# Performance work log

Hardware: AMD Instinct MI355X
Metric: run time of the kernel (lower is better)

Reference implementation:

```python
import jax, jax.numpy as jnp
import numpy as np


def _iir_forward(b_coeff, rho, psi, u_in, y_init, u_init):
    # Coefficient computation: stable 2nd-order resonator parameterization
    r = jax.nn.sigmoid(rho)
    theta = jnp.pi * jax.nn.sigmoid(psi)
    a1 = -2.0 * r * jnp.cos(theta)
    a2 = r * r

    B, T = u_in.shape
    nb = b_coeff.shape[0]  # number of FIR taps (n_b)

    # FIR (moving-average) part, fully vectorized over batch and time:
    # v[t] = sum_k b[k] * u[t-k]; past inputs come from u_init = [u[-1], u[-2], ...]
    u_ext = jnp.concatenate([u_init[:, ::-1], u_in], axis=1)  # [B, T + nb - 1], time-ordered
    v = jnp.zeros_like(u_in)
    for k in range(nb):  # small fixed loop over filter taps
        v = v + b_coeff[k] * jax.lax.dynamic_slice_in_dim(u_ext, nb - 1 - k, T, axis=1)

    # AR (recursive) part: y[t] = v[t] - a1*y[t-1] - a2*y[t-2]  (sequential scan over time)
    def step(carry, v_t):
        y1, y2 = carry  # y[t-1], y[t-2], each [B]
        y = v_t - a1 * y1 - a2 * y2
        return (y, y1), y

    init = (y_init[:, 0], y_init[:, 1])  # [y[-1], y[-2]] per lfiltic convention
    _, y = jax.lax.scan(step, init, v.T)  # y: [T, B]
    return y.T  # [B, T]


def setup_inputs() -> dict:
    key = jax.random.key(0)
    k1, k2, k3, k4 = jax.random.split(key, 4)
    B, T, NB = 1024, 16384, 3
    return {
        "b_coeff": 0.1 * jax.random.normal(k1, (NB,), dtype=jnp.float32),
        "rho": jnp.asarray(jax.random.normal(k2, (), dtype=jnp.float32) + 0.9),
        "psi": jnp.asarray(jax.random.normal(k3, (), dtype=jnp.float32) * 0.5),
        "u_in": jax.random.normal(k4, (B, T), dtype=jnp.float32),
        "y_init": jnp.zeros((B, 2), dtype=jnp.float32),
        "u_init": jnp.zeros((B, NB - 1), dtype=jnp.float32),
    }


def reference(b_coeff, rho, psi, u_in, y_init, u_init):
    return _iir_forward(b_coeff, rho, psi, u_in, y_init, u_init)
```

## Files before the change

kernel.cpp:

```cpp
#include <hip/hip_runtime.h>
#include <math.h>


#define TLEN  16384
#define HALF  8192
#define NT    256
#define CK    32
#define NCH   256
#define CARRY (2*NCH)

__device__ __forceinline__ void mat2_sq(float& m00, float& m01, float& m10, float& m11) {
    float t00 = m00*m00 + m01*m10;
    float t01 = m00*m01 + m01*m11;
    float t10 = m10*m00 + m11*m10;
    float t11 = m10*m01 + m11*m11;
    m00 = t00; m01 = t01; m10 = t10; m11 = t11;
}

__global__ __launch_bounds__(NT, 4)
void iir_kernel(const float* __restrict__ bc,
                const float* __restrict__ rho_p,
                const float* __restrict__ psi_p,
                const float* __restrict__ u_in,
                const float* __restrict__ y_init,
                const float* __restrict__ u_init,
                float* __restrict__ y_out)
{
    __shared__ float sc[2*NCH + 2];
    const int row = blockIdx.x;
    const int tid = threadIdx.x;

    const float rho = rho_p[0];
    const float psi = psi_p[0];
    const float r   = 1.0f / (1.0f + expf(-rho));
    const float th  = 3.14159265358979323846f / (1.0f + expf(-psi));
    const float a1  = -2.0f * r * cosf(th);
    const float a2  = r * r;
    const float b0  = bc[0], b1 = bc[1], b2 = bc[2];

    const float* urow = u_in  + (size_t)row * TLEN;
    float*       orow = y_out + (size_t)row * TLEN;

    for (int h = 0; h < 2; ++h) {
        const float* uc0 = urow + h * HALF + CK * tid;

        float um2, um1;
        if (tid == 0 && h == 0) {
            um2 = u_init[2*row + 1];
            um1 = u_init[2*row + 0];
        } else {
            float2 ub = *(const float2*)(uc0 - 2);
            um2 = ub.x; um1 = ub.y;
        }

        float uu[CK];
        #pragma unroll
        for (int k = 0; k < CK/4; ++k)
            *(float4*)&uu[4*k] = ((const float4*)uc0)[k];

        float v[CK];
        float y1 = 0.0f, y2 = 0.0f;
        #pragma unroll
        for (int j = 0; j < CK; ++j) {
            float uc = uu[j];
            float vv = fmaf(b2, um2, fmaf(b1, um1, b0 * uc));
            v[j] = vv;
            float y = fmaf(-a1, y1, fmaf(-a2, y2, vv));
            y2 = y1; y1 = y;
            um2 = um1; um1 = uc;
        }
        sc[2*tid]     = y1;
        sc[2*tid + 1] = y2;
        __syncthreads();

        if (tid < 64) {
            const int l = tid;
            float m00 = -a1, m01 = -a2, m10 = 1.0f, m11 = 0.0f;
            #pragma unroll
            for (int s = 0; s < 5; ++s) mat2_sq(m00, m01, m10, m11);

            float da[4], db[4];
            #pragma unroll
            for (int m = 0; m < 4; ++m) {
                da[m] = sc[8*l + 2*m];
                db[m] = sc[8*l + 2*m + 1];
            }

            float seed0 = 0.0f, seed1 = 0.0f;
            if (l == 0) {
                if (h == 0) { seed0 = y_init[2*row]; seed1 = y_init[2*row + 1]; }
                else        { seed0 = sc[CARRY]; seed1 = sc[CARRY + 1]; }
            }
            float s0 = seed0, s1 = seed1;
            #pragma unroll
            for (int m = 0; m < 4; ++m) {
                float n0 = fmaf(m00, s0, fmaf(m01, s1, da[m]));
                float n1 = fmaf(m10, s0, fmaf(m11, s1, db[m]));
                s0 = n0; s1 = n1;
            }
            float w00 = m00, w01 = m01, w10 = m10, w11 = m11;
            mat2_sq(w00, w01, w10, w11);
            mat2_sq(w00, w01, w10, w11);
            #pragma unroll
            for (int p = 0; p < 6; ++p) {
                float o0 = __shfl_up(s0, 1 << p);
                float o1 = __shfl_up(s1, 1 << p);
                if (l >= (1 << p)) {
                    s0 = fmaf(w00, o0, fmaf(w01, o1, s0));
                    s1 = fmaf(w10, o0, fmaf(w11, o1, s1));
                }
                if (p < 5) mat2_sq(w00, w01, w10, w11);
            }
            float p0 = __shfl_up(s0, 1);
            float p1 = __shfl_up(s1, 1);
            if (l == 0) { p0 = seed0; p1 = seed1; }
            float c0 = p0, c1 = p1;
            #pragma unroll
            for (int m = 0; m < 4; ++m) {
                sc[2*(4*l + m)]     = c0;
                sc[2*(4*l + m) + 1] = c1;
                float n0 = fmaf(m00, c0, fmaf(m01, c1, da[m]));
                float n1 = fmaf(m10, c0, fmaf(m11, c1, db[m]));
                c0 = n0; c1 = n1;
            }
        }
        __syncthreads();

        float y1f = sc[2*tid];
        float y2f = sc[2*tid + 1];
        float* oc0 = orow + h * HALF + CK * tid;
        float yy[CK];
        #pragma unroll
        for (int j = 0; j < CK; ++j) {
            float y = fmaf(-a1, y1f, fmaf(-a2, y2f, v[j]));
            yy[j] = y;
            y2f = y1f; y1f = y;
        }
        #pragma unroll
        for (int k = 0; k < CK/4; ++k)
            ((float4*)oc0)[k] = *(const float4*)&yy[4*k];

        if (tid == NT - 1) {
            sc[CARRY]     = y1f;
            sc[CARRY + 1] = y2f;
        }
    }
}

extern "C" void kernel_launch(void* const* d_in, const int* in_sizes, int n_in,
                              void* d_out, int out_size, void* d_ws, size_t ws_size,
                              hipStream_t stream) {
    const float* bc    = (const float*)d_in[0];
    const float* rho   = (const float*)d_in[1];
    const float* psi   = (const float*)d_in[2];
    const float* u_in  = (const float*)d_in[3];
    const float* y_in  = (const float*)d_in[4];
    const float* u_ini = (const float*)d_in[5];
    float* y = (float*)d_out;
    const int B = in_sizes[3] / TLEN;
    iir_kernel<<<B, NT, 0, stream>>>(bc, rho, psi, u_in, y_in, u_ini, y);
}
```

Before: 133.5 us.

## Stage loads through padded per-wave LDS, use wave-level scan, and prefetch second half

Each wave now owns a contiguous 2048-element segment and stages global loads and stores through a padded per-wave LDS region, so global accesses become coalesced float4 streams instead of per-thread 128-byte strided chunks. The single-wave scan over all 256 chunk states is replaced by a wave-local shuffle scan in every wave plus a short 4-step cross-wave combine, and the per-lane matrix prefix powers are precomputed once. The second half's input is prefetched into registers while the first half computes. The cost is more registers (staged float4 buffer, matrices), extra LDS traffic, and reliance on __threadfence_block rather than barriers for intra-wave LDS visibility.

After: 146.6 us. 9.8% more time.

```diff
diff --git a/kernel.cpp b/kernel.cpp
--- a/kernel.cpp
+++ b/kernel.cpp
@@ -5,16 +5,21 @@
 #define TLEN  16384
 #define HALF  8192
 #define NT    256
-#define CK    32
-#define NCH   256
-#define CARRY (2*NCH)
+#define NW    4
+#define SEG   2048
+#define WPAD  2304
+#define SUMS  (NW * WPAD)
+#define CARRY (SUMS + 16)
+#define LDSF  (CARRY + 2)
 
-__device__ __forceinline__ void mat2_sq(float& m00, float& m01, float& m10, float& m11) {
-    float t00 = m00*m00 + m01*m10;
-    float t01 = m00*m01 + m01*m11;
-    float t10 = m10*m00 + m11*m10;
-    float t11 = m10*m01 + m11*m11;
-    m00 = t00; m01 = t01; m10 = t10; m11 = t11;
+struct M2 { float a, b, c, d; };
+__device__ __forceinline__ M2 mmul(const M2& x, const M2& y) {
+    M2 r;
+    r.a = fmaf(x.a, y.a, x.b * y.c);
+    r.b = fmaf(x.a, y.b, x.b * y.d);
+    r.c = fmaf(x.c, y.a, x.d * y.c);
+    r.d = fmaf(x.c, y.b, x.d * y.d);
+    return r;
 }
 
 __global__ __launch_bounds__(NT, 4)
@@ -26,9 +31,12 @@
                 const float* __restrict__ u_init,
                 float* __restrict__ y_out)
 {
-    __shared__ float sc[2*NCH + 2];
+    __shared__ __align__(16) float lds[LDSF];
     const int row = blockIdx.x;
     const int tid = threadIdx.x;
+    const int w   = tid >> 6;
+    const int l   = tid & 63;
+    float* wreg = lds + w * WPAD;
 
     const float rho = rho_p[0];
     const float psi = psi_p[0];
@@ -38,30 +46,55 @@
     const float a2  = r * r;
     const float b0  = bc[0], b1 = bc[1], b2 = bc[2];
 
+    M2 M = { -a1, -a2, 1.0f, 0.0f };
+    #pragma unroll
+    for (int s = 0; s < 5; ++s) M = mmul(M, M);
+    M2 W = M, P = { 1.0f, 0.0f, 0.0f, 1.0f };
+    #pragma unroll
+    for (int p = 0; p < 6; ++p) {
+        if ((l >> p) & 1) P = mmul(W, P);
+        W = mmul(W, W);
+    }
+    const M2 Mseg = W;
+
     const float* urow = u_in  + (size_t)row * TLEN;
     float*       orow = y_out + (size_t)row * TLEN;
 
+    float4 st[8];
+    {
+        const float4* us = (const float4*)(urow + w * SEG);
+        #pragma unroll
+        for (int k = 0; k < 8; ++k) st[k] = us[l + 64 * k];
+    }
+
     for (int h = 0; h < 2; ++h) {
-        const float* uc0 = urow + h * HALF + CK * tid;
+        #pragma unroll
+        for (int k = 0; k < 8; ++k) {
+            int g = l + 64 * k;
+            *(float4*)&wreg[4 * (g + (g >> 3))] = st[k];
+        }
+        __threadfence_block();
+
+        float uu[32];
+        #pragma unroll
+        for (int j = 0; j < 8; ++j)
+            *(float4*)&uu[4 * j] = *(const float4*)&wreg[4 * (9 * l + j)];
 
         float um2, um1;
-        if (tid == 0 && h == 0) {
-            um2 = u_init[2*row + 1];
-            um1 = u_init[2*row + 0];
-        } else {
-            float2 ub = *(const float2*)(uc0 - 2);
-            um2 = ub.x; um1 = ub.y;
+        {
+            float pm2 = __shfl_up(uu[30], 1);
+            float pm1 = __shfl_up(uu[31], 1);
+            if (l == 0) {
+                int gstart = h * HALF + w * SEG;
+                if (gstart == 0) { um2 = u_init[2 * row + 1]; um1 = u_init[2 * row + 0]; }
+                else { float2 b = *(const float2*)(urow + gstart - 2); um2 = b.x; um1 = b.y; }
+            } else { um2 = pm2; um1 = pm1; }
         }
 
-        float uu[CK];
-        #pragma unroll
-        for (int k = 0; k < CK/4; ++k)
-            *(float4*)&uu[4*k] = ((const float4*)uc0)[k];
-
-        float v[CK];
+        float v[32];
         float y1 = 0.0f, y2 = 0.0f;
         #pragma unroll
-        for (int j = 0; j < CK; ++j) {
+        for (int j = 0; j < 32; ++j) {
             float uc = uu[j];
             float vv = fmaf(b2, um2, fmaf(b1, um1, b0 * uc));
             v[j] = vv;
@@ -69,80 +102,72 @@
             y2 = y1; y1 = y;
             um2 = um1; um1 = uc;
         }
-        sc[2*tid]     = y1;
-        sc[2*tid + 1] = y2;
-        __syncthreads();
 
-        if (tid < 64) {
-            const int l = tid;
-            float m00 = -a1, m01 = -a2, m10 = 1.0f, m11 = 0.0f;
+        if (h == 0) {
+            const float4* us = (const float4*)(urow + HALF + w * SEG);
             #pragma unroll
-            for (int s = 0; s < 5; ++s) mat2_sq(m00, m01, m10, m11);
+            for (int k = 0; k < 8; ++k) st[k] = us[l + 64 * k];
+        }
 
-            float da[4], db[4];
-            #pragma unroll
-            for (int m = 0; m < 4; ++m) {
-                da[m] = sc[8*l + 2*m];
-                db[m] = sc[8*l + 2*m + 1];
-            }
-
-            float seed0 = 0.0f, seed1 = 0.0f;
-            if (l == 0) {
-                if (h == 0) { seed0 = y_init[2*row]; seed1 = y_init[2*row + 1]; }
-                else        { seed0 = sc[CARRY]; seed1 = sc[CARRY + 1]; }
-            }
-            float s0 = seed0, s1 = seed1;
-            #pragma unroll
-            for (int m = 0; m < 4; ++m) {
-                float n0 = fmaf(m00, s0, fmaf(m01, s1, da[m]));
-                float n1 = fmaf(m10, s0, fmaf(m11, s1, db[m]));
+        float s0 = y1, s1 = y2;
+        M2 Wp = M;
+        #pragma unroll
+        for (int p = 0; p < 6; ++p) {
+            float o0 = __shfl_up(s0, 1 << p);
+            float o1 = __shfl_up(s1, 1 << p);
+            if (l >= (1 << p)) {
+                float n0 = fmaf(Wp.a, o0, fmaf(Wp.b, o1, s0));
+                float n1 = fmaf(Wp.c, o0, fmaf(Wp.d, o1, s1));
                 s0 = n0; s1 = n1;
             }
-            float w00 = m00, w01 = m01, w10 = m10, w11 = m11;
-            mat2_sq(w00, w01, w10, w11);
-            mat2_sq(w00, w01, w10, w11);
-            #pragma unroll
-            for (int p = 0; p < 6; ++p) {
-                float o0 = __shfl_up(s0, 1 << p);
-                float o1 = __shfl_up(s1, 1 << p);
-                if (l >= (1 << p)) {
-                    s0 = fmaf(w00, o0, fmaf(w01, o1, s0));
-                    s1 = fmaf(w10, o0, fmaf(w11, o1, s1));
-                }
-                if (p < 5) mat2_sq(w00, w01, w10, w11);
-            }
-            float p0 = __shfl_up(s0, 1);
-            float p1 = __shfl_up(s1, 1);
-            if (l == 0) { p0 = seed0; p1 = seed1; }
-            float c0 = p0, c1 = p1;
-            #pragma unroll
-            for (int m = 0; m < 4; ++m) {
-                sc[2*(4*l + m)]     = c0;
-                sc[2*(4*l + m) + 1] = c1;
-                float n0 = fmaf(m00, c0, fmaf(m01, c1, da[m]));
-                float n1 = fmaf(m10, c0, fmaf(m11, c1, db[m]));
-                c0 = n0; c1 = n1;
-            }
+            if (p < 5) Wp = mmul(Wp, Wp);
+        }
+        float e0 = __shfl_up(s0, 1);
+        float e1 = __shfl_up(s1, 1);
+        if (l == 0) { e0 = 0.0f; e1 = 0.0f; }
+
+        if (l == 63) {
+            lds[SUMS + 8 * h + 2 * w]     = s0;
+            lds[SUMS + 8 * h + 2 * w + 1] = s1;
         }
         __syncthreads();
 
-        float y1f = sc[2*tid];
-        float y2f = sc[2*tid + 1];
-        float* oc0 = orow + h * HALF + CK * tid;
-        float yy[CK];
+        float t0, t1;
+        if (h == 0) { t0 = y_init[2 * row]; t1 = y_init[2 * row + 1]; }
+        else        { t0 = lds[CARRY]; t1 = lds[CARRY + 1]; }
+        float c0 = t0, c1 = t1;
         #pragma unroll
-        for (int j = 0; j < CK; ++j) {
-            float y = fmaf(-a1, y1f, fmaf(-a2, y2f, v[j]));
-            yy[j] = y;
-            y2f = y1f; y1f = y;
+        for (int j = 0; j < NW; ++j) {
+            float q0 = lds[SUMS + 8 * h + 2 * j];
+            float q1 = lds[SUMS + 8 * h + 2 * j + 1];
+            float n0 = fmaf(Mseg.a, c0, fmaf(Mseg.b, c1, q0));
+            float n1 = fmaf(Mseg.c, c0, fmaf(Mseg.d, c1, q1));
+            c0 = n0; c1 = n1;
+            if (j == w - 1) { t0 = c0; t1 = c1; }
         }
+        if (h == 0 && tid == 0) { lds[CARRY] = c0; lds[CARRY + 1] = c1; }
+
+        float in0 = fmaf(P.a, t0, fmaf(P.b, t1, e0));
+        float in1 = fmaf(P.c, t0, fmaf(P.d, t1, e1));
+
+        float py1 = in0, py2 = in1;
         #pragma unroll
-        for (int k = 0; k < CK/4; ++k)
-            ((float4*)oc0)[k] = *(const float4*)&yy[4*k];
+        for (int j = 0; j < 8; ++j) {
+            float x0 = fmaf(-a1, py1, fmaf(-a2, py2, v[4 * j + 0]));
+            float x1 = fmaf(-a1, x0,  fmaf(-a2, py1, v[4 * j + 1]));
+            float x2 = fmaf(-a1, x1,  fmaf(-a2, x0,  v[4 * j + 2]));
+            float x3 = fmaf(-a1, x2,  fmaf(-a2, x1,  v[4 * j + 3]));
+            float4 q; q.x = x0; q.y = x1; q.z = x2; q.w = x3;
+            *(float4*)&wreg[4 * (9 * l + j)] = q;
+            py2 = x2; py1 = x3;
+        }
+        __threadfence_block();
 
-        if (tid == NT - 1) {
-            sc[CARRY]     = y1f;
-            sc[CARRY + 1] = y2f;
+        float4* os = (float4*)(orow + h * HALF + w * SEG);
+        #pragma unroll
+        for (int k = 0; k < 8; ++k) {
+            int g = l + 64 * k;
+            os[g] = *(const float4*)&wreg[4 * (g + (g >> 3))];
         }
     }
 }
```
